# Optimization experiments

Measured on AMD Instinct MI355X. Metric: run time of the kernel, lower is better.

## Reference

```python
import jax, jax.numpy as jnp
import numpy as np

B, T, C, H = 2, 2048, 1024, 16
D = C // H  # head dim = 64

def setup_inputs() -> dict:
    key = jax.random.key(0)
    ks = jax.random.split(key, 5)
    s = 1.0 / np.sqrt(C)
    return {
        "x": jax.random.normal(ks[0], (B, T, C), jnp.float32),
        "Wq": jax.random.normal(ks[1], (C, C), jnp.float32) * s,
        "Wk": jax.random.normal(ks[2], (C, C), jnp.float32) * s,
        "Wv": jax.random.normal(ks[3], (C, C), jnp.float32) * s,
        "Wo": jax.random.normal(ks[4], (C, C), jnp.float32) * s,
    }

def reference(x, Wq, Wk, Wv, Wo):
    # torch Linear: y = x @ W.T  (weights stored [out, in])
    def proj(W):
        h = jnp.einsum('btc,oc->bto', x, W)
        return h.reshape(B, T, H, D).transpose(0, 2, 1, 3)  # [B,H,T,D]
    q, k, v = proj(Wq), proj(Wk), proj(Wv)
    scale = 1.0 / np.sqrt(D)
    att = jnp.einsum('bhqd,bhkd->bhqk', q, k) * scale  # [B,H,T,T]
    causal = jnp.tril(jnp.ones((T, T), bool))
    att = jnp.where(causal[None, None], att, -jnp.inf)
    att = jax.nn.softmax(att, axis=-1)
    y = jnp.einsum('bhqk,bhkd->bhqd', att, v)  # [B,H,T,D]
    y = y.transpose(0, 2, 1, 3).reshape(B, T, C)
    return jnp.einsum('btc,oc->bto', y, Wo)
```

## Files before the change

kernel.cpp:

```cpp
#include <hip/hip_runtime.h>
#include <math.h>

typedef short bf16x8 __attribute__((ext_vector_type(8)));
typedef float f32x4 __attribute__((ext_vector_type(4)));
typedef float f32x16 __attribute__((ext_vector_type(16)));
typedef int int2v __attribute__((ext_vector_type(2)));

constexpr int Bc = 2, Tc = 2048, Cc = 1024, Hc = 16, Dc = 64;
constexpr int Mc = Bc * Tc;

#if __has_builtin(__builtin_amdgcn_exp2f)
#define EXP2(x) __builtin_amdgcn_exp2f(x)
#else
#define EXP2(x) exp2f(x)
#endif

__device__ __forceinline__ unsigned short f2bf(float f) {
    union { float f; unsigned u; } v; v.f = f;
    unsigned r = v.u + 0x7fffu + ((v.u >> 16) & 1u);
    return (unsigned short)(r >> 16);
}

__device__ __forceinline__ float bf2f(unsigned short u) {
    union { unsigned u; float f; } v; v.u = (unsigned)u << 16; return v.f;
}

__device__ __forceinline__ unsigned cvt_pk_bf16(float lo, float hi) {
    unsigned r;
    asm("v_cvt_pk_bf16_f32 %0, %1, %2" : "=v"(r) : "v"(lo), "v"(hi));
    return r;
}

__device__ __forceinline__ void gload16(const void* g, void* l) {
    __builtin_amdgcn_global_load_lds(
        (const __attribute__((address_space(1))) void*)g,
        (__attribute__((address_space(3))) void*)l, 16, 0, 0);
}

__global__ __launch_bounds__(256)
void cast_bf16(const float* __restrict__ in, unsigned short* __restrict__ out, int n8) {
    int i = blockIdx.x * 256 + threadIdx.x;
    if (i >= n8) return;
    const float4* p = (const float4*)in;
    float4 a = p[i * 2], b = p[i * 2 + 1];
    union { unsigned short u[8]; bf16x8 v; } r;
    r.u[0] = f2bf(a.x); r.u[1] = f2bf(a.y); r.u[2] = f2bf(a.z); r.u[3] = f2bf(a.w);
    r.u[4] = f2bf(b.x); r.u[5] = f2bf(b.y); r.u[6] = f2bf(b.z); r.u[7] = f2bf(b.w);
    *(bf16x8*)(out + i * 8) = r.v;
}

__global__ __launch_bounds__(256)
void cast_w4(const float* __restrict__ a, const float* __restrict__ b,
             const float* __restrict__ c, const float* __restrict__ d,
             unsigned short* __restrict__ oa, unsigned short* __restrict__ ob,
             unsigned short* __restrict__ oc, unsigned short* __restrict__ od) {
    const float* src = blockIdx.y == 0 ? a : blockIdx.y == 1 ? b : blockIdx.y == 2 ? c : d;
    unsigned short* dst = blockIdx.y == 0 ? oa : blockIdx.y == 1 ? ob : blockIdx.y == 2 ? oc : od;
    int i = blockIdx.x * 256 + threadIdx.x;
    const float4* p = (const float4*)src;
    float4 x = p[i * 2], y = p[i * 2 + 1];
    union { unsigned short u[8]; bf16x8 v; } r;
    r.u[0] = f2bf(x.x); r.u[1] = f2bf(x.y); r.u[2] = f2bf(x.z); r.u[3] = f2bf(x.w);
    r.u[4] = f2bf(y.x); r.u[5] = f2bf(y.y); r.u[6] = f2bf(y.z); r.u[7] = f2bf(y.w);
    *(bf16x8*)(dst + i * 8) = r.v;
}

__global__ __launch_bounds__(256)
void gemm_qkv(const unsigned short* __restrict__ A,
              const unsigned short* __restrict__ Wq,
              const unsigned short* __restrict__ Wk,
              const unsigned short* __restrict__ Wv,
              unsigned short* __restrict__ Qo,
              unsigned short* __restrict__ Ko,
              unsigned short* __restrict__ Vo) {
    __shared__ unsigned short As[128 * 32];
    __shared__ unsigned short Bs[128 * 32];
    const int t = threadIdx.x;
    const int lane = t & 63, l15 = lane & 15, l4 = lane >> 4;
    const int w = t >> 6, wr = w >> 1, wc = w & 1;
    const int seg = blockIdx.y >> 3;
    const unsigned short* W = seg == 0 ? Wq : seg == 1 ? Wk : Wv;
    const int m0 = blockIdx.x * 128, n0 = (blockIdx.y & 7) * 128;

    f32x4 acc[4][4] = {};

    for (int k0 = 0; k0 < Cc; k0 += 32) {
        __syncthreads();
        #pragma unroll
        for (int it = 0; it < 2; ++it) {
            int c = t + it * 256;
            int row = c >> 2, ko = (c & 3) << 3;
            gload16(A + (size_t)(m0 + row) * Cc + k0 + ko, As + c * 8);
            gload16(W + (size_t)(n0 + row) * Cc + k0 + ko, Bs + c * 8);
        }
        __syncthreads();
        bf16x8 af[4], bfr[4];
        #pragma unroll
        for (int i = 0; i < 4; ++i)
            af[i] = *(const bf16x8*)(As + ((wr * 64 + i * 16 + l15) * 32 + l4 * 8));
        #pragma unroll
        for (int j = 0; j < 4; ++j)
            bfr[j] = *(const bf16x8*)(Bs + ((wc * 64 + j * 16 + l15) * 32 + l4 * 8));
        #pragma unroll
        for (int i = 0; i < 4; ++i)
            #pragma unroll
            for (int j = 0; j < 4; ++j)
                acc[i][j] = __builtin_amdgcn_mfma_f32_16x16x32_bf16(af[i], bfr[j], acc[i][j], 0, 0, 0);
    }

    const float qscale = 0.18033688011112042f;
    const int r0 = wr * 64 + (l4 << 2);
    const int c0 = wc * 64 + l15;
    #pragma unroll
    for (int i = 0; i < 4; ++i)
        #pragma unroll
        for (int j = 0; j < 4; ++j)
            #pragma unroll
            for (int r = 0; r < 4; ++r) {
                int row = m0 + r0 + i * 16 + r;
                int col = n0 + c0 + j * 16;
                float v = acc[i][j][r];
                int bb = row >> 11, tt = row & (Tc - 1);
                int hh = col >> 6, dd = col & 63;
                if (seg == 0)
                    Qo[((((size_t)bb * Hc + hh) * Tc + tt) << 6) + dd] = f2bf(v * qscale);
                else if (seg == 1)
                    Ko[((((size_t)bb * Hc + hh) * Tc + tt) << 6) + dd] = f2bf(v);
                else
                    Vo[(((size_t)bb * Hc + hh) * Dc + dd) * Tc + tt] = f2bf(v);
            }
}

__global__ __launch_bounds__(256)
void gemm_out(const unsigned short* __restrict__ A,
              const unsigned short* __restrict__ W,
              float* __restrict__ outp) {
    __shared__ unsigned short As[128 * 32];
    __shared__ unsigned short Bs[64 * 32];
    const int t = threadIdx.x;
    const int lane = t & 63, l15 = lane & 15, l4 = lane >> 4;
    const int w = t >> 6, wr = w >> 1, wc = w & 1;
    const int m0 = blockIdx.x * 128, n0 = blockIdx.y * 64;

    f32x4 acc[4][2] = {};

    for (int k0 = 0; k0 < Cc; k0 += 32) {
        __syncthreads();
        #pragma unroll
        for (int it = 0; it < 2; ++it) {
            int c = t + it * 256;
            int row = c >> 2, ko = (c & 3) << 3;
            gload16(A + (size_t)(m0 + row) * Cc + k0 + ko, As + c * 8);
        }
        {
            int c = t;
            int row = c >> 2, ko = (c & 3) << 3;
            gload16(W + (size_t)(n0 + row) * Cc + k0 + ko, Bs + c * 8);
        }
        __syncthreads();
        bf16x8 af[4], bfr[2];
        #pragma unroll
        for (int i = 0; i < 4; ++i)
            af[i] = *(const bf16x8*)(As + ((wr * 64 + i * 16 + l15) * 32 + l4 * 8));
        #pragma unroll
        for (int j = 0; j < 2; ++j)
            bfr[j] = *(const bf16x8*)(Bs + ((wc * 32 + j * 16 + l15) * 32 + l4 * 8));
        #pragma unroll
        for (int i = 0; i < 4; ++i)
            #pragma unroll
            for (int j = 0; j < 2; ++j)
                acc[i][j] = __builtin_amdgcn_mfma_f32_16x16x32_bf16(af[i], bfr[j], acc[i][j], 0, 0, 0);
    }

    const int r0 = wr * 64 + (l4 << 2);
    const int c0 = wc * 32 + l15;
    #pragma unroll
    for (int i = 0; i < 4; ++i)
        #pragma unroll
        for (int j = 0; j < 2; ++j)
            #pragma unroll
            for (int r = 0; r < 4; ++r)
                outp[(size_t)(m0 + r0 + i * 16 + r) * Cc + n0 + c0 + j * 16] = acc[i][j][r];
}

__device__ __constant__ unsigned char JOBS[48] = {
    159, 223, 222, 15, 158, 157, 221, 220, 14, 156,
    155, 219, 218, 13, 154, 153, 217, 216, 12, 152,
    151, 215, 214, 11, 150, 149, 213, 212, 10, 148,
    147, 211, 210,  9, 146, 145, 209, 208,  8, 144,
      7,   6,   5,  4,   3,   2,   1,   0
};

__global__ __launch_bounds__(128)
void attn_mfma(const unsigned short* __restrict__ Q,
               const unsigned short* __restrict__ K,
               const unsigned short* __restrict__ Vt,
               unsigned short* __restrict__ Y,
               unsigned short* __restrict__ P1,
               float* __restrict__ mlf) {
    __shared__ unsigned short Ks[2][64 * 64];
    __shared__ unsigned short Vs[2][64 * 64];

    const int t = threadIdx.x, lane = t & 63, w = t >> 6;
    const int l31 = lane & 31, h = lane >> 5;
    const int bh = blockIdx.x;
    const int bb = bh >> 4, hh = bh & 15;

    const unsigned char job = JOBS[blockIdx.y];
    const int c = job & 31;
    const bool split = job & 128;
    const int half = (job >> 6) & 1;
    const int ntile = c + 1, smid = ntile >> 1;
    const int kb0 = (split && half) ? smid : 0;
    const int kb1 = (split && !half) ? smid : ntile;

    const int qbase = c * 64 + w * 32;
    const int q = qbase + l31;

    const unsigned short* Qp = Q + (size_t)bh * Tc * Dc;
    const unsigned short* Kp = K + (size_t)bh * Tc * Dc;
    const unsigned short* Vp = Vt + (size_t)bh * Dc * Tc;

    bf16x8 qf[4];
    #pragma unroll
    for (int kc = 0; kc < 4; ++kc)
        qf[kc] = *(const bf16x8*)(Qp + (size_t)q * 64 + kc * 16 + h * 8);

    f32x16 ot[2] = {};
    float m = -INFINITY, lsum = 0.f;

    auto stage = [&](int kb, int buf) {
        #pragma unroll
        for (int it = 0; it < 4; ++it) {
            int idx = t + it * 128;
            int row = idx >> 3, slot = idx & 7;
            int ss = slot ^ (row & 7);
            gload16(Kp + (size_t)(kb * 64 + row) * 64 + ss * 8, &Ks[buf][idx * 8]);
            gload16(Vp + (size_t)row * Tc + kb * 64 + ss * 8, &Vs[buf][idx * 8]);
        }
    };

    stage(kb0, 0);
    __syncthreads();

    for (int kb = kb0; kb < kb1; ++kb) {
        const int cur = (kb - kb0) & 1;
        if (kb + 1 < kb1) stage(kb + 1, cur ^ 1);

        f32x16 st[2] = {};
        __builtin_amdgcn_s_setprio(1);
        #pragma unroll
        for (int nt = 0; nt < 2; ++nt) {
            int key = nt * 32 + l31;
            #pragma unroll
            for (int kc = 0; kc < 4; ++kc) {
                int boff = (kc * 32 + h * 16) ^ ((key & 7) << 4);
                bf16x8 kf = *(const bf16x8*)(&Ks[cur][((key << 7) + boff) >> 1]);
                st[nt] = __builtin_amdgcn_mfma_f32_32x32x16_bf16(kf, qf[kc], st[nt], 0, 0, 0);
            }
        }
        __builtin_amdgcn_s_setprio(0);

        if (kb * 64 + 63 > qbase) {
            #pragma unroll
            for (int nt = 0; nt < 2; ++nt)
                #pragma unroll
                for (int r = 0; r < 16; ++r) {
                    int key = kb * 64 + nt * 32 + (r & 3) + 8 * (r >> 2) + 4 * h;
                    if (key > q) st[nt][r] = -1e30f;
                }
        }

        float mx[16];
        #pragma unroll
        for (int r = 0; r < 16; ++r) mx[r] = fmaxf(st[0][r], st[1][r]);
        #pragma unroll
        for (int s2 = 8; s2 > 0; s2 >>= 1)
            #pragma unroll
            for (int r = 0; r < s2; ++r) mx[r] = fmaxf(mx[r], mx[r + s2]);
        float tmax = fmaxf(mx[0], __shfl_xor(mx[0], 32));

        if (__any(tmax > m + 8.f)) {
            float mn = fmaxf(m, tmax);
            float al = EXP2(m - mn);
            m = mn;
            lsum *= al;
            #pragma unroll
            for (int dt = 0; dt < 2; ++dt)
                #pragma unroll
                for (int r = 0; r < 16; ++r) ot[dt][r] *= al;
        }

        float psa[4] = {0.f, 0.f, 0.f, 0.f};
        #pragma unroll
        for (int nt = 0; nt < 2; ++nt)
            #pragma unroll
            for (int r = 0; r < 16; ++r) {
                float p = EXP2(st[nt][r] - m);
                st[nt][r] = p;
                psa[r & 3] += p;
            }
        lsum += (psa[0] + psa[1]) + (psa[2] + psa[3]);

        #pragma unroll
        for (int nt = 0; nt < 2; ++nt) {
            unsigned a0 = cvt_pk_bf16(st[nt][0],  st[nt][1]);
            unsigned b0 = cvt_pk_bf16(st[nt][4],  st[nt][5]);
            unsigned a1 = cvt_pk_bf16(st[nt][2],  st[nt][3]);
            unsigned b1 = cvt_pk_bf16(st[nt][6],  st[nt][7]);
            int2v r0 = __builtin_amdgcn_permlane32_swap((int)a0, (int)b0, false, false);
            int2v r1 = __builtin_amdgcn_permlane32_swap((int)a1, (int)b1, false, false);
            union { unsigned u[4]; bf16x8 v; } pf0, pf1;
            pf0.u[0] = r0.x; pf0.u[1] = r1.x; pf0.u[2] = r0.y; pf0.u[3] = r1.y;
            unsigned c0 = cvt_pk_bf16(st[nt][8],  st[nt][9]);
            unsigned d0 = cvt_pk_bf16(st[nt][12], st[nt][13]);
            unsigned c1 = cvt_pk_bf16(st[nt][10], st[nt][11]);
            unsigned d1 = cvt_pk_bf16(st[nt][14], st[nt][15]);
            int2v r2 = __builtin_amdgcn_permlane32_swap((int)c0, (int)d0, false, false);
            int2v r3 = __builtin_amdgcn_permlane32_swap((int)c1, (int)d1, false, false);
            pf1.u[0] = r2.x; pf1.u[1] = r3.x; pf1.u[2] = r2.y; pf1.u[3] = r3.y;

            __builtin_amdgcn_s_setprio(1);
            #pragma unroll
            for (int dt = 0; dt < 2; ++dt) {
                int d = dt * 32 + l31;
                int v0off = (nt * 64 + h * 16) ^ ((d & 7) << 4);
                bf16x8 vf0 = *(const bf16x8*)(&Vs[cur][((d << 7) + v0off) >> 1]);
                ot[dt] = __builtin_amdgcn_mfma_f32_32x32x16_bf16(vf0, pf0.v, ot[dt], 0, 0, 0);
            }
            #pragma unroll
            for (int dt = 0; dt < 2; ++dt) {
                int d = dt * 32 + l31;
                int v1off = (nt * 64 + 32 + h * 16) ^ ((d & 7) << 4);
                bf16x8 vf1 = *(const bf16x8*)(&Vs[cur][((d << 7) + v1off) >> 1]);
                ot[dt] = __builtin_amdgcn_mfma_f32_32x32x16_bf16(vf1, pf1.v, ot[dt], 0, 0, 0);
            }
            __builtin_amdgcn_s_setprio(0);
        }
        __syncthreads();
    }

    float lf = lsum + __shfl_xor(lsum, 32);
    unsigned short* dst = (split && half) ? P1 : Y;
    float inv = split ? 1.f : 1.f / lf;
    size_t base = ((size_t)bb * Tc + q) * Cc + hh * 64;
    #pragma unroll
    for (int dt = 0; dt < 2; ++dt)
        #pragma unroll
        for (int rg = 0; rg < 4; ++rg) {
            int d0 = dt * 32 + rg * 8 + 4 * h;
            ushort4 s4;
            s4.x = f2bf(ot[dt][rg * 4 + 0] * inv);
            s4.y = f2bf(ot[dt][rg * 4 + 1] * inv);
            s4.z = f2bf(ot[dt][rg * 4 + 2] * inv);
            s4.w = f2bf(ot[dt][rg * 4 + 3] * inv);
            *(ushort4*)(dst + base + d0) = s4;
        }
    if (split && h == 0) {
        int ridx = bh * 1024 + (q - 1024);
        mlf[ridx + (half ? 65536 : 0)]          = m;
        mlf[ridx + (half ? 98304 : 32768)]      = lf;
    }
}

__global__ __launch_bounds__(256)
void attn_combine(unsigned short* __restrict__ Y,
                  const unsigned short* __restrict__ P1,
                  const float* __restrict__ mlf) {
    int tid = blockIdx.x * 256 + threadIdx.x;
    int ridx = tid >> 3;
    int d0 = (tid & 7) * 8;
    int bh = ridx >> 10, qq = ridx & 1023;
    int bb = bh >> 4, hh = bh & 15;
    int q = 1024 + qq;
    size_t off = ((size_t)bb * Tc + q) * Cc + hh * 64 + d0;
    float m0 = mlf[ridx], l0 = mlf[ridx + 32768];
    float m1 = mlf[ridx + 65536], l1 = mlf[ridx + 98304];
    float M = fmaxf(m0, m1);
    float a0 = exp2f(m0 - M), a1 = exp2f(m1 - M);
    float inv = 1.f / (l0 * a0 + l1 * a1);
    union { unsigned short u[8]; bf16x8 v; } y0, y1, r;
    y0.v = *(const bf16x8*)(Y + off);
    y1.v = *(const bf16x8*)(P1 + off);
    #pragma unroll
    for (int j = 0; j < 8; ++j)
        r.u[j] = f2bf((bf2f(y0.u[j]) * a0 + bf2f(y1.u[j]) * a1) * inv);
    *(bf16x8*)(Y + off) = r.v;
}

extern "C" void kernel_launch(void* const* d_in, const int* in_sizes, int n_in,
                              void* d_out, int out_size, void* d_ws, size_t ws_size,
                              hipStream_t stream) {
    const float* x  = (const float*)d_in[0];
    const float* Wq = (const float*)d_in[1];
    const float* Wk = (const float*)d_in[2];
    const float* Wv = (const float*)d_in[3];
    const float* Wo = (const float*)d_in[4];

    unsigned short* ws = (unsigned short*)d_ws;
    const size_t nX = (size_t)Mc * Cc;
    const size_t nW = (size_t)Cc * Cc;
    size_t off = 0;
    unsigned short* xb  = ws + off; off += nX;
    unsigned short* Wqb = ws + off; off += nW;
    unsigned short* Wkb = ws + off; off += nW;
    unsigned short* Wvb = ws + off; off += nW;
    unsigned short* Wob = ws + off; off += nW;
    unsigned short* Qw  = ws + off; off += nX;
    unsigned short* Kw  = ws + off; off += nX;
    unsigned short* Vtw = ws + off; off += nX;
    unsigned short* Yb  = ws + off; off += nX;

    dim3 blk(256);
    cast_bf16<<<dim3((int)(nX / 8 / 256)), blk, 0, stream>>>(x, xb, (int)(nX / 8));
    cast_w4<<<dim3(512, 4), blk, 0, stream>>>(Wq, Wk, Wv, Wo, Wqb, Wkb, Wvb, Wob);

    gemm_qkv<<<dim3(Mc / 128, 24), blk, 0, stream>>>(xb, Wqb, Wkb, Wvb, Qw, Kw, Vtw);

    unsigned short* P1 = xb;
    float* mlf = (float*)Wqb;
    attn_mfma<<<dim3(Bc * Hc, 48), dim3(128), 0, stream>>>(Qw, Kw, Vtw, Yb, P1, mlf);
    attn_combine<<<dim3(1024), blk, 0, stream>>>(Yb, P1, mlf);

    gemm_out<<<dim3(Mc / 128, Cc / 64), blk, 0, stream>>>(Yb, Wob, (float*)d_out);
}
```

Baseline: 117.9 us.

## Double-buffer GEMM LDS tiles and use explicit vmcnt waits for async prefetch

Converts both projection GEMMs from single-buffered LDS staging with two full syncthreads per k-step into a two-deep ring. The next tiles are issued ahead and waited on with explicit s_waitcnt vmcnt counts plus raw s_barrier. The attention kernel gets the same restructuring, with two blocks prefetched up front and the refill issued after the compute barrier. MFMA sections are wrapped in s_setprio. This is meant to hide global-to-LDS latency behind MFMA work, at the cost of doubled LDS use and fragile hand-counted vmcnt values that must match the number of outstanding loads.

```diff
diff --git a/kernel.cpp b/kernel.cpp
--- a/kernel.cpp
+++ b/kernel.cpp
@@ -14,6 +14,10 @@
 #else
 #define EXP2(x) exp2f(x)
 #endif
+
+#define SBAR() do { asm volatile("" ::: "memory"); \
+                    __builtin_amdgcn_s_barrier();   \
+                    asm volatile("" ::: "memory"); } while (0)
 
 __device__ __forceinline__ unsigned short f2bf(float f) {
     union { float f; unsigned u; } v; v.f = f;
@@ -73,8 +77,8 @@
               unsigned short* __restrict__ Qo,
               unsigned short* __restrict__ Ko,
               unsigned short* __restrict__ Vo) {
-    __shared__ unsigned short As[128 * 32];
-    __shared__ unsigned short Bs[128 * 32];
+    __shared__ unsigned short As[2][128 * 32];
+    __shared__ unsigned short Bs[2][128 * 32];
     const int t = threadIdx.x;
     const int lane = t & 63, l15 = lane & 15, l4 = lane >> 4;
     const int w = t >> 6, wr = w >> 1, wc = w & 1;
@@ -84,28 +88,44 @@
 
     f32x4 acc[4][4] = {};
 
-    for (int k0 = 0; k0 < Cc; k0 += 32) {
-        __syncthreads();
+    auto stageg = [&](int kk, int buf) {
+        int k0 = kk * 32;
         #pragma unroll
         for (int it = 0; it < 2; ++it) {
             int c = t + it * 256;
             int row = c >> 2, ko = (c & 3) << 3;
-            gload16(A + (size_t)(m0 + row) * Cc + k0 + ko, As + c * 8);
-            gload16(W + (size_t)(n0 + row) * Cc + k0 + ko, Bs + c * 8);
-        }
-        __syncthreads();
+            gload16(A + (size_t)(m0 + row) * Cc + k0 + ko, As[buf] + c * 8);
+            gload16(W + (size_t)(n0 + row) * Cc + k0 + ko, Bs[buf] + c * 8);
+        }
+    };
+
+    const int NK = Cc / 32;
+    stageg(0, 0);
+    stageg(1, 1);
+
+    for (int kk = 0; kk < NK; ++kk) {
+        const int cur = kk & 1;
+        if (kk + 1 < NK) asm volatile("s_waitcnt vmcnt(4)" ::: "memory");
+        else             asm volatile("s_waitcnt vmcnt(0)" ::: "memory");
+        SBAR();
+
         bf16x8 af[4], bfr[4];
         #pragma unroll
         for (int i = 0; i < 4; ++i)
-            af[i] = *(const bf16x8*)(As + ((wr * 64 + i * 16 + l15) * 32 + l4 * 8));
+            af[i] = *(const bf16x8*)(As[cur] + ((wr * 64 + i * 16 + l15) * 32 + l4 * 8));
         #pragma unroll
         for (int j = 0; j < 4; ++j)
-            bfr[j] = *(const bf16x8*)(Bs + ((wc * 64 + j * 16 + l15) * 32 + l4 * 8));
+            bfr[j] = *(const bf16x8*)(Bs[cur] + ((wc * 64 + j * 16 + l15) * 32 + l4 * 8));
+        __builtin_amdgcn_s_setprio(1);
         #pragma unroll
         for (int i = 0; i < 4; ++i)
             #pragma unroll
             for (int j = 0; j < 4; ++j)
                 acc[i][j] = __builtin_amdgcn_mfma_f32_16x16x32_bf16(af[i], bfr[j], acc[i][j], 0, 0, 0);
+        __builtin_amdgcn_s_setprio(0);
+
+        SBAR();
+        if (kk + 2 < NK) stageg(kk + 2, cur);
     }
 
     const float qscale = 0.18033688011112042f;
@@ -135,8 +155,8 @@
 void gemm_out(const unsigned short* __restrict__ A,
               const unsigned short* __restrict__ W,
               float* __restrict__ outp) {
-    __shared__ unsigned short As[128 * 32];
-    __shared__ unsigned short Bs[64 * 32];
+    __shared__ unsigned short As[2][128 * 32];
+    __shared__ unsigned short Bs[2][64 * 32];
     const int t = threadIdx.x;
     const int lane = t & 63, l15 = lane & 15, l4 = lane >> 4;
     const int w = t >> 6, wr = w >> 1, wc = w & 1;
@@ -144,32 +164,47 @@
 
     f32x4 acc[4][2] = {};
 
-    for (int k0 = 0; k0 < Cc; k0 += 32) {
-        __syncthreads();
+    auto stageg = [&](int kk, int buf) {
+        int k0 = kk * 32;
         #pragma unroll
         for (int it = 0; it < 2; ++it) {
             int c = t + it * 256;
             int row = c >> 2, ko = (c & 3) << 3;
-            gload16(A + (size_t)(m0 + row) * Cc + k0 + ko, As + c * 8);
+            gload16(A + (size_t)(m0 + row) * Cc + k0 + ko, As[buf] + c * 8);
         }
         {
-            int c = t;
-            int row = c >> 2, ko = (c & 3) << 3;
-            gload16(W + (size_t)(n0 + row) * Cc + k0 + ko, Bs + c * 8);
-        }
-        __syncthreads();
+            int row = t >> 2, ko = (t & 3) << 3;
+            gload16(W + (size_t)(n0 + row) * Cc + k0 + ko, Bs[buf] + t * 8);
+        }
+    };
+
+    const int NK = Cc / 32;
+    stageg(0, 0);
+    stageg(1, 1);
+
+    for (int kk = 0; kk < NK; ++kk) {
+        const int cur = kk & 1;
+        if (kk + 1 < NK) asm volatile("s_waitcnt vmcnt(3)" ::: "memory");
+        else             asm volatile("s_waitcnt vmcnt(0)" ::: "memory");
+        SBAR();
+
         bf16x8 af[4], bfr[2];
         #pragma unroll
         for (int i = 0; i < 4; ++i)
-            af[i] = *(const bf16x8*)(As + ((wr * 64 + i * 16 + l15) * 32 + l4 * 8));
+            af[i] = *(const bf16x8*)(As[cur] + ((wr * 64 + i * 16 + l15) * 32 + l4 * 8));
         #pragma unroll
         for (int j = 0; j < 2; ++j)
-            bfr[j] = *(const bf16x8*)(Bs + ((wc * 32 + j * 16 + l15) * 32 + l4 * 8));
+            bfr[j] = *(const bf16x8*)(Bs[cur] + ((wc * 32 + j * 16 + l15) * 32 + l4 * 8));
+        __builtin_amdgcn_s_setprio(1);
         #pragma unroll
         for (int i = 0; i < 4; ++i)
             #pragma unroll
             for (int j = 0; j < 2; ++j)
                 acc[i][j] = __builtin_amdgcn_mfma_f32_16x16x32_bf16(af[i], bfr[j], acc[i][j], 0, 0, 0);
+        __builtin_amdgcn_s_setprio(0);
+
+        SBAR();
+        if (kk + 2 < NK) stageg(kk + 2, cur);
     }
 
     const int r0 = wr * 64 + (l4 << 2);
@@ -241,11 +276,13 @@
     };
 
     stage(kb0, 0);
-    __syncthreads();
+    if (kb0 + 1 < kb1) stage(kb0 + 1, 1);
 
     for (int kb = kb0; kb < kb1; ++kb) {
         const int cur = (kb - kb0) & 1;
-        if (kb + 1 < kb1) stage(kb + 1, cur ^ 1);
+        if (kb + 1 < kb1) asm volatile("s_waitcnt vmcnt(8)" ::: "memory");
+        else              asm volatile("s_waitcnt vmcnt(0)" ::: "memory");
+        SBAR();
 
         f32x16 st[2] = {};
         __builtin_amdgcn_s_setprio(1);
@@ -337,7 +374,9 @@
             }
             __builtin_amdgcn_s_setprio(0);
         }
-        __syncthreads();
+
+        SBAR();
+        if (kb + 2 < kb1) stage(kb + 2, cur);
     }
 
     float lf = lsum + __shfl_xor(lsum, 32);
@@ -358,8 +397,8 @@
         }
     if (split && h == 0) {
         int ridx = bh * 1024 + (q - 1024);
-        mlf[ridx + (half ? 65536 : 0)]          = m;
-        mlf[ridx + (half ? 98304 : 32768)]      = lf;
+        mlf[ridx + (half ? 65536 : 0)]     = m;
+        mlf[ridx + (half ? 98304 : 32768)] = lf;
     }
 }
 
```

After: 123.6 us. +4.8%, slower.
